# Performance work log

Hardware: AMD Instinct MI355X
Metric: run time of the kernel (lower is better)

The kernel has to match this reference:

```python
import jax, jax.numpy as jnp
import numpy as np


def mT(x):
    return jnp.swapaxes(x, -1, -2)


def bmv(A, x):
    # batched matrix-vector with broadcasting over leading dims
    return jnp.einsum('...mn,...n->...m', A, x)


def tri_inv(chol):
    # inverse of a batched lower-triangular matrix
    n = chol.shape[-1]
    I = jnp.broadcast_to(jnp.eye(n, dtype=chol.dtype), chol.shape)
    return jax.scipy.linalg.solve_triangular(chol, I, lower=True)


def chol_solve(Psi, v):
    # (chol chol^T)^{-1} v where Psi = inv(chol)^T  =>  Psi Psi^T v
    return bmv(Psi, bmv(mT(Psi), v))


def setup_inputs() -> dict:
    T, S, B, L, r = 500, 32, 128, 64, 8
    key = jax.random.key(0)
    ks = jax.random.split(key, 11)
    m_0 = jax.random.normal(ks[0], (L,), dtype=jnp.float32)
    Q_0_diag = 0.1 + 0.9 * jax.random.uniform(ks[1], (L,), dtype=jnp.float32)
    Q_diag = 0.1 + 0.9 * jax.random.uniform(ks[2], (L,), dtype=jnp.float32)
    k = 0.1 * jax.random.normal(ks[3], (T, B, L), dtype=jnp.float32)
    K = 0.3 * jax.random.normal(ks[4], (T, B, L, r), dtype=jnp.float32)
    A = jax.random.normal(ks[5], (L, L), dtype=jnp.float32) / jnp.sqrt(jnp.float32(L))
    w_p0 = jax.random.normal(ks[6], (S, B, L), dtype=jnp.float32)
    w_f0 = jax.random.normal(ks[7], (S, B, r), dtype=jnp.float32)
    w_p1 = jax.random.normal(ks[8], (T - 1, S, B, S), dtype=jnp.float32)
    w_p2 = jax.random.normal(ks[9], (T - 1, S, B, L), dtype=jnp.float32)
    w_f = jax.random.normal(ks[10], (T - 1, S, B, r), dtype=jnp.float32)
    return dict(m_0=m_0, Q_0_diag=Q_0_diag, Q_diag=Q_diag, k=k, K=K, A=A,
                w_p0=w_p0, w_f0=w_f0, w_p1=w_p1, w_p2=w_p2, w_f=w_f)


def reference(m_0, Q_0_diag, Q_diag, k, K, A, w_p0, w_f0, w_p1, w_p2, w_f):
    S = w_p0.shape[0]
    r = K.shape[-1]
    Qi = 1.0 / Q_diag
    Qs = jnp.sqrt(Q_diag)
    I_r = jnp.eye(r, dtype=K.dtype)
    I_S = jnp.eye(S, dtype=K.dtype)
    sqrt_S_inv = 1.0 / jnp.sqrt(jnp.asarray(S, K.dtype))

    def dyn(z):  # nonlinear dynamics mean fn (stand-in): residual tanh network
        return z + 0.1 * jnp.tanh(z @ A.T)

    # ---- fast_filter_step_0 ----
    Pp = Q_0_diag                               # initial predictive cov diag [L]
    z_p_c = jnp.sqrt(Pp) * w_p0                 # [S,B,L]
    h_p = jnp.broadcast_to(m_0 / Pp, k[0].shape)  # J_p m_p, [B,L]
    h = h_p + k[0]
    P_p_K = Pp[None, :, None] * K[0]            # [B,L,r]
    KPK = jnp.einsum('blr,bls->brs', K[0], P_p_K)
    Psi0 = mT(tri_inv(jnp.linalg.cholesky(I_r + KPK)))
    m0f = Pp * h - bmv(P_p_K, chol_solve(Psi0, bmv(mT(P_p_K), h)))
    v1 = bmv(mT(K[0]), z_p_c) + w_f0            # [S,B,r]
    z0 = m0f + z_p_c - Pp * bmv(K[0], chol_solve(Psi0, v1))

    # ---- fast_filter_step_t over t = 1..T-1 ----
    def step(z_f, xs):
        k_t, K_t, wp1, wp2, wf = xs
        # predict
        mth = jnp.moveaxis(dyn(z_f), 0, -1)     # [B,L,S]
        m_p = mth.mean(-1)                      # [B,L]
        M_c = sqrt_S_inv * (mth - m_p[..., None])  # [B,L,S]
        G = (mT(M_c) * Qi) @ M_c                # [B,S,S]
        Psi_p = mT(tri_inv(jnp.linalg.cholesky(I_S + G)))
        u1 = Qi * m_p
        h_p = u1 - Qi * bmv(M_c, chol_solve(Psi_p, bmv(mT(M_c), u1)))  # J_p m_p
        z_p_c = bmv(M_c, wp1) + Qs * wp2        # [S,B,L]
        # update
        h = h_p + k_t
        KM = mT(K_t) @ M_c                      # [B,r,S]
        KQ = mT(K_t) * Qs                       # [B,r,L]
        KPK_t = KM @ mT(KM) + KQ @ mT(KQ)
        Psi_f = mT(tri_inv(jnp.linalg.cholesky(I_r + KPK_t)))

        def P_p_mv(v):
            return bmv(M_c, bmv(mT(M_c), v)) + Q_diag * v

        u = P_p_mv(h)
        m_f = u - P_p_mv(bmv(K_t, chol_solve(Psi_f, bmv(mT(K_t), u))))
        v1t = bmv(mT(K_t), z_p_c) + wf
        z = m_f + z_p_c - P_p_mv(bmv(K_t, chol_solve(Psi_f, v1t)))
        return z, m_f

    _, m_rest = jax.lax.scan(step, z0, (k[1:], K[1:], w_p1, w_p2, w_f))
    return jnp.concatenate([m0f[None], m_rest], axis=0)  # [T,B,L]
```

## Files before the change

kernel.cpp:

```cpp
#include <hip/hip_runtime.h>
#include <hip/hip_bf16.h>
#include <cstdint>
#include <cstddef>

namespace {
constexpr int T_ = 500, S_ = 32, B_ = 128, L_ = 64, R_ = 8;

typedef __attribute__((ext_vector_type(8))) short short8;
typedef __attribute__((ext_vector_type(4))) float f32x4;

__device__ __forceinline__ float rdlane(float v, int l) {
  return __int_as_float(__builtin_amdgcn_readlane(__float_as_int(v), l));
}
template<int CTRL, int RM>
__device__ __forceinline__ float dppadd(float v) {
  int t = __builtin_amdgcn_update_dpp(0, __float_as_int(v), CTRL, RM, 0xf, false);
  return v + __int_as_float(t);
}
__device__ __forceinline__ float wredsum(float v) {
  v = dppadd<0x111, 0xf>(v);
  v = dppadd<0x112, 0xf>(v);
  v = dppadd<0x114, 0xf>(v);
  v = dppadd<0x118, 0xf>(v);
  v = dppadd<0x142, 0xa>(v);
  v = dppadd<0x143, 0xc>(v);
  return v;
}
__device__ __forceinline__ float wsum(float v) {
  v += __shfl_xor(v, 1);  v += __shfl_xor(v, 2);  v += __shfl_xor(v, 4);
  v += __shfl_xor(v, 8);  v += __shfl_xor(v, 16); v += __shfl_xor(v, 32);
  return v;
}
__device__ __forceinline__ void gload16(const float* g, float* l) {
  __builtin_amdgcn_global_load_lds((const __attribute__((address_space(1))) uint32_t*)g,
                                   (__attribute__((address_space(3))) uint32_t*)l,
                                   16, 0, 0);
}
__device__ __forceinline__ void bar_lgkm() {
  asm volatile("s_waitcnt lgkmcnt(0)\n\ts_barrier" ::: "memory");
}
__device__ __forceinline__ void fsplit(const float (&v)[8], short8& hi, short8& lo) {
#pragma unroll
  for (int j = 0; j < 8; ++j) {
    uint32_t u = __float_as_uint(v[j]);
    hi[j] = (short)(u >> 16);
    float hf = __uint_as_float(u & 0xFFFF0000u);
    float lf = v[j] - hf;
    lo[j] = (short)(__float_as_uint(lf) >> 16);
  }
}
__device__ __forceinline__ void ldfragF(const float* p, short8& hi, short8& lo) {
  float4 a = *(const float4*)p, b = *(const float4*)(p + 4);
  float v[8] = {a.x,a.y,a.z,a.w,b.x,b.y,b.z,b.w};
  fsplit(v, hi, lo);
}
__device__ __forceinline__ f32x4 mfma3(short8 ah, short8 al, short8 bh, short8 bl,
                                       f32x4 acc) {
  acc = __builtin_amdgcn_mfma_f32_16x16x32_bf16(ah, bh, acc, 0, 0, 0);
  acc = __builtin_amdgcn_mfma_f32_16x16x32_bf16(al, bh, acc, 0, 0, 0);
  acc = __builtin_amdgcn_mfma_f32_16x16x32_bf16(ah, bl, acc, 0, 0, 0);
  return acc;
}
}

__global__ __launch_bounds__(512, 1) void nlf_kernel(
    const float* __restrict__ m0p, const float* __restrict__ q0p,
    const float* __restrict__ qp,  const float* __restrict__ kp,
    const float* __restrict__ Kp,  const float* __restrict__ Ap,
    const float* __restrict__ wp0p, const float* __restrict__ wf0p,
    const float* __restrict__ wp1p, const float* __restrict__ wp2p,
    const float* __restrict__ wfp,  float* __restrict__ outp)
{
  __shared__ __align__(16) float z_s[S_*68];
  __shared__ __align__(16) float zn_s[S_*68];
  __shared__ __align__(16) float Mc_s[L_*36];
  __shared__ __align__(16) short McH_s[L_*40];
  __shared__ __align__(16) short McL_s[L_*40];
  __shared__ __align__(16) short McTH_s[S_*72];
  __shared__ __align__(16) short McTL_s[S_*72];
  __shared__ __align__(16) short KtTH_s[R_*72];
  __shared__ __align__(16) short KtTL_s[R_*72];
  __shared__ __align__(16) float uni[8*68];
  __shared__ __align__(16) float wp1b[2][S_*S_];
  __shared__ __align__(16) float wp2b[2][S_*L_];
  __shared__ __align__(16) float wf_s[S_*R_];
  __shared__ __align__(16) float Ktb[2][L_*R_];
  __shared__ __align__(16) float KtT_s[R_*68];
  __shared__ __align__(16) float ktv_s[L_];
  __shared__ __align__(16) float v1t_s[S_*R_];
  __shared__ __align__(16) float KM_s[S_*R_];
  __shared__ __align__(16) float mkm_s[L_*R_];
  __shared__ __align__(16) float M8_s[64];
  __shared__ __align__(16) float C8_s[64];
  __shared__ __align__(16) float tk_s[S_];
  __shared__ __align__(16) float mf_s[L_];
  __shared__ __align__(16) float qv_s[L_];
  __shared__ __align__(16) float qsv_s[L_];
  __shared__ __align__(16) float q0v_s[L_];

  const int tid = threadIdx.x;
  const int lam = tid & 63;
  const int w   = tid >> 6;
  const int b   = blockIdx.x;
  const int mtl = w >> 2, ntl = w & 3;
  const int cc  = lam & 15, gg = lam >> 4;

  const float q_r  = qp[lam];
  const float qs_r = sqrtf(q_r);
  const float q0_r = q0p[lam];
  const float m0_r = m0p[lam];
  if (tid < 64) { qv_s[tid] = q_r; qsv_s[tid] = qs_r; q0v_s[tid] = q0_r; }

  short8 ABh[2], ABl[2];
  {
    const float* arow = Ap + (size_t)(ntl*16 + cc)*64;
#pragma unroll
    for (int kk = 0; kk < 2; ++kk)
      ldfragF(arow + kk*32 + gg*8, ABh[kk], ABl[kk]);
  }

  float Kreg[8];
  {
    const float* kb = Kp + (size_t)b*(L_*R_) + lam*R_;
    float4 ka = *(const float4*)kb, kb4 = *(const float4*)(kb+4);
    Kreg[0]=ka.x;Kreg[1]=ka.y;Kreg[2]=ka.z;Kreg[3]=ka.w;
    Kreg[4]=kb4.x;Kreg[5]=kb4.y;Kreg[6]=kb4.z;Kreg[7]=kb4.w;
  }
  float kt_r = kp[(size_t)b*L_ + lam];

  if (w == 0) {
#pragma unroll
    for (int m = 0; m < 4; ++m) {
      int f = m*256 + lam*4, s = f >> 5, c = f & 31;
      gload16(wp1p + ((size_t)s*B_ + b)*S_ + c, &wp1b[1][f]);
    }
  } else if (w == 1 || w == 2) {
#pragma unroll
    for (int m = 0; m < 4; ++m) {
      int f = (w-1)*1024 + m*256 + lam*4, s = f >> 6, c = f & 63;
      gload16(wp2p + ((size_t)s*B_ + b)*L_ + c, &wp2b[1][f]);
    }
  } else if (w == 3) {
    { int f = lam*4, s = f >> 3, c = f & 7;
      gload16(wf0p + ((size_t)s*B_ + b)*R_ + c, &wf_s[f]); }
#pragma unroll
    for (int m = 0; m < 2; ++m) {
      int f = m*256 + lam*4;
      gload16(Kp + (size_t)b*(L_*R_) + f, &Ktb[0][f]);
    }
  } else if (w == 4 || w == 5) {
#pragma unroll
    for (int m = 0; m < 4; ++m) {
      int f = (w-4)*1024 + m*256 + lam*4, s = f >> 6, c = f & 63;
      gload16(wp0p + ((size_t)s*B_ + b)*L_ + c, &wp2b[0][f]);
    }
  } else if (w == 6) {
#pragma unroll
    for (int m = 0; m < 2; ++m) {
      int f = m*256 + lam*4;
      gload16(Kp + ((size_t)1*B_ + b)*(L_*R_) + f, &Ktb[1][f]);
    }
  }
  __syncthreads();

  auto chol8M8 = [&]() {
    const int i8 = lam & 7;
    float c8[8], rd8 = 0.0f;
#pragma unroll
    for (int k = 0; k < 8; ++k) c8[k] = C8_s[i8*8 + k];
#pragma unroll
    for (int j = 0; j < 8; ++j) {
      float dj = rdlane(c8[j], j);
      float rinv = rsqrtf(dj);
      if (i8 == j) rd8 = rinv;
      c8[j] *= rinv;
#pragma unroll
      for (int k = j+1; k < 8; ++k)
        c8[k] = fmaf(-rdlane(c8[j], k), c8[j], c8[k]);
    }
    float w8[8];
#pragma unroll
    for (int i = 0; i < 8; ++i) {
      float sacc = (i == i8) ? 1.0f : 0.0f;
#pragma unroll
      for (int k = 0; k < i; ++k)
        sacc = fmaf(-rdlane(c8[k], i), w8[k], sacc);
      w8[i] = sacc * rdlane(rd8, i);
    }
#pragma unroll
    for (int i = 0; i < 8; ++i) {
      float msum = 0.0f;
#pragma unroll
      for (int k = 0; k < 8; ++k)
        msum = fmaf(rdlane(w8[k], i), w8[k], msum);
      if (lam < 8) M8_s[i*8 + lam] = msum;
    }
  };

  {
    const float Pp = q0_r;
    const float h0 = m0_r / Pp + kt_r;
    if (w == 0) {
      const int r1 = lam >> 3, r2 = lam & 7;
      float acc = 0.0f;
#pragma unroll 4
      for (int l = 0; l < 64; ++l)
        acc = fmaf(Ktb[0][l*8 + r1] * q0v_s[l], Ktb[0][l*8 + r2], acc);
      C8_s[lam] = acc + (r1 == r2 ? 1.0f : 0.0f);
      chol8M8();
      float t8[8];
#pragma unroll
      for (int r = 0; r < 8; ++r) t8[r] = wsum(Pp * Kreg[r] * h0);
      float acc2 = 0.0f;
#pragma unroll
      for (int r1i = 0; r1i < 8; ++r1i) {
        float4 ma = *(const float4*)&M8_s[r1i*8];
        float4 mb = *(const float4*)&M8_s[r1i*8+4];
        float y = ma.x*t8[0]+ma.y*t8[1]+ma.z*t8[2]+ma.w*t8[3]
                + mb.x*t8[4]+mb.y*t8[5]+mb.z*t8[6]+mb.w*t8[7];
        acc2 = fmaf(Kreg[r1i], y, acc2);
      }
      float m0f = Pp*h0 - Pp*acc2;
      mf_s[lam] = m0f;
      outp[(size_t)b*L_ + lam] = m0f;
    }
    __syncthreads();

    const float qs0 = sqrtf(q0_r);
#pragma unroll
    for (int i = 0; i < 4; ++i) {
      const int s = 4*w + i;
      float zp = qs0 * wp2b[0][s*64 + lam];
      float v1[8];
#pragma unroll
      for (int r = 0; r < 8; ++r)
        v1[r] = wsum(Kreg[r] * zp) + wf_s[s*8 + r];
      float acc = 0.0f;
#pragma unroll
      for (int r1i = 0; r1i < 8; ++r1i) {
        float4 ma = *(const float4*)&M8_s[r1i*8];
        float4 mb = *(const float4*)&M8_s[r1i*8+4];
        float y = ma.x*v1[0]+ma.y*v1[1]+ma.z*v1[2]+ma.w*v1[3]
                + mb.x*v1[4]+mb.y*v1[5]+mb.z*v1[6]+mb.w*v1[7];
        acc = fmaf(Kreg[r1i], y, acc);
      }
      z_s[s*68 + lam] = zp - Pp*acc;
    }
  }
  __syncthreads();

  for (int t = 1; t < T_; ++t) {
    const int cb = t & 1, nb = cb ^ 1;

    {
      const float* kb = Kp + ((size_t)t*B_ + b)*(L_*R_) + lam*R_;
      float4 ka = *(const float4*)kb, kb4 = *(const float4*)(kb+4);
      Kreg[0]=ka.x;Kreg[1]=ka.y;Kreg[2]=ka.z;Kreg[3]=ka.w;
      Kreg[4]=kb4.x;Kreg[5]=kb4.y;Kreg[6]=kb4.z;Kreg[7]=kb4.w;
      kt_r = kp[((size_t)t*B_ + b)*L_ + lam];
    }
    if (w == 0) ktv_s[lam] = kt_r;

    {
      f32x4 acc = {0.0f, 0.0f, 0.0f, 0.0f};
#pragma unroll
      for (int kk = 0; kk < 2; ++kk) {
        const int l0 = kk*32 + gg*8;
        const int row = mtl*16 + cc;
        float4 za = *(const float4*)&z_s[row*68 + l0];
        float4 zb = *(const float4*)&z_s[row*68 + l0 + 4];
        float4 ma4 = *(const float4*)&mf_s[l0];
        float4 mb4 = *(const float4*)&mf_s[l0 + 4];
        float z8[8] = {za.x+ma4.x, za.y+ma4.y, za.z+ma4.z, za.w+ma4.w,
                       zb.x+mb4.x, zb.y+mb4.y, zb.z+mb4.z, zb.w+mb4.w};
        short8 ah, al;
        fsplit(z8, ah, al);
        acc = __builtin_amdgcn_mfma_f32_16x16x32_bf16(ah, ABh[kk], acc, 0, 0, 0);
        acc = __builtin_amdgcn_mfma_f32_16x16x32_bf16(al, ABh[kk], acc, 0, 0, 0);
        acc = __builtin_amdgcn_mfma_f32_16x16x32_bf16(ah, ABl[kk], acc, 0, 0, 0);
      }
      const int lout = ntl*16 + cc;
      const float mfl = mf_s[lout];
      float psum = 0.0f;
#pragma unroll
      for (int r = 0; r < 4; ++r) {
        const int sr = mtl*16 + gg*4 + r;
        float x = acc[r];
        float e = __expf(2.0f*x);
        float tnh = 1.0f - 2.0f/(e + 1.0f);
        float zv = (z_s[sr*68 + lout] + mfl) + 0.1f*tnh;
        zn_s[sr*68 + lout] = zv;
        psum += zv;
      }
      uni[(mtl*4 + gg)*68 + lout] = psum;
    }
    bar_lgkm();

    if (w == 0) {
      if (t < T_-1) {
#pragma unroll
        for (int m = 0; m < 4; ++m) {
          int f = m*256 + lam*4, s = f >> 5, c = f & 31;
          gload16(wp1p + (((size_t)t*S_ + s)*B_ + b)*S_ + c, &wp1b[nb][f]);
        }
      }
    } else if (w == 1 || w == 2) {
      if (t < T_-1) {
#pragma unroll
        for (int m = 0; m < 4; ++m) {
          int f = (w-1)*1024 + m*256 + lam*4, s = f >> 6, c = f & 63;
          gload16(wp2p + (((size_t)t*S_ + s)*B_ + b)*L_ + c, &wp2b[nb][f]);
        }
      }
    } else if (w == 3) {
      { int f = lam*4, s = f >> 3, c = f & 7;
        gload16(wfp + (((size_t)(t-1)*S_ + s)*B_ + b)*R_ + c, &wf_s[f]); }
      if (t < T_-1) {
#pragma unroll
        for (int m = 0; m < 2; ++m) {
          int f = m*256 + lam*4;
          gload16(Kp + ((size_t)(t+1)*B_ + b)*(L_*R_) + f, &Ktb[nb][f]);
        }
      }
    }

    float mp = 0.0f;
#pragma unroll
    for (int ww = 0; ww < 8; ++ww) mp += uni[ww*68 + lam];
    mp *= 0.03125f;
    {
      short h4[4], l4[4];
#pragma unroll
      for (int i = 0; i < 4; ++i) {
        const int s = 4*w + i;
        float mcv = (zn_s[s*68 + lam] - mp) * 0.17677669529663689f;
        Mc_s[lam*36 + s] = mcv;
        uint32_t u = __float_as_uint(mcv);
        short hs = (short)(u >> 16);
        float hf = __uint_as_float(u & 0xFFFF0000u);
        short ls = (short)(__float_as_uint(mcv - hf) >> 16);
        h4[i] = hs; l4[i] = ls;
        McTH_s[s*72 + lam] = hs;
        McTL_s[s*72 + lam] = ls;
      }
      uint32_t hp0 = (uint32_t)(uint16_t)h4[0] | ((uint32_t)(uint16_t)h4[1] << 16);
      uint32_t hp1 = (uint32_t)(uint16_t)h4[2] | ((uint32_t)(uint16_t)h4[3] << 16);
      uint32_t lp0 = (uint32_t)(uint16_t)l4[0] | ((uint32_t)(uint16_t)l4[1] << 16);
      uint32_t lp1 = (uint32_t)(uint16_t)l4[2] | ((uint32_t)(uint16_t)l4[3] << 16);
      *(uint2*)&McH_s[lam*40 + 4*w] = make_uint2(hp0, hp1);
      *(uint2*)&McL_s[lam*40 + 4*w] = make_uint2(lp0, lp1);
    }
    if (w == 5) {
      float4 a = *(const float4*)&Ktb[cb][lam*8];
      float4 c4 = *(const float4*)&Ktb[cb][lam*8+4];
      float kv[8] = {a.x,a.y,a.z,a.w,c4.x,c4.y,c4.z,c4.w};
#pragma unroll
      for (int r = 0; r < 8; ++r) {
        KtT_s[r*68 + lam] = kv[r];
        uint32_t u = __float_as_uint(kv[r]);
        short hs = (short)(u >> 16);
        float hf = __uint_as_float(u & 0xFFFF0000u);
        short ls = (short)(__float_as_uint(kv[r] - hf) >> 16);
        KtTH_s[r*72 + lam] = hs;
        KtTL_s[r*72 + lam] = ls;
      }
    }
    __syncthreads();

    if (w >= 2) {
      auto zpTile = [&](int tl) {
        const int mt = tl >> 2, nt = tl & 3;
        short8 ah, al;
        ldfragF(&wp1b[cb][(mt*16+cc)*32 + gg*8], ah, al);
        short8 bh = *(const short8*)&McH_s[(nt*16+cc)*40 + gg*8];
        short8 bl = *(const short8*)&McL_s[(nt*16+cc)*40 + gg*8];
        f32x4 acc = {0,0,0,0};
        acc = mfma3(ah, al, bh, bl, acc);
        const int col = nt*16 + cc;
        const float qsc = qsv_s[col];
#pragma unroll
        for (int r = 0; r < 4; ++r) {
          const int row = mt*16 + gg*4 + r;
          zn_s[row*68 + col] = acc[r] + qsc * wp2b[cb][row*64 + col];
        }
      };
      if (w <= 5) zpTile(w - 2);
      else { zpTile(2*w - 8); zpTile(2*w - 7); }
    } else {
      const int mt = w;
      f32x4 acc = {0,0,0,0};
#pragma unroll
      for (int ks = 0; ks < 2; ++ks) {
        short8 ah = *(const short8*)&McTH_s[(mt*16+cc)*72 + ks*32 + gg*8];
        short8 al = *(const short8*)&McTL_s[(mt*16+cc)*72 + ks*32 + gg*8];
        short8 bh, bl;
        if (cc < 8) {
          bh = *(const short8*)&KtTH_s[cc*72 + ks*32 + gg*8];
          bl = *(const short8*)&KtTL_s[cc*72 + ks*32 + gg*8];
        } else if (cc == 8) {
          float bv[8];
#pragma unroll
          for (int j = 0; j < 8; ++j) bv[j] = ktv_s[ks*32 + gg*8 + j];
          fsplit(bv, bh, bl);
        } else {
          bh = short8{0,0,0,0,0,0,0,0}; bl = short8{0,0,0,0,0,0,0,0};
        }
        acc = mfma3(ah, al, bh, bl, acc);
      }
#pragma unroll
      for (int r = 0; r < 4; ++r) {
        const int s = mt*16 + gg*4 + r;
        if (cc < 8) KM_s[s*8 + cc] = acc[r];
        else if (cc == 8) tk_s[s] = acc[r];
      }
    }
    bar_lgkm();

    float u_r = 0.0f, t8s[8];
#pragma unroll
    for (int r = 0; r < 8; ++r) t8s[r] = 0.0f;
    if (w == 0) {
      float mctk = 0.0f;
#pragma unroll
      for (int s4 = 0; s4 < 32; s4 += 4) {
        float4 mc4 = *(const float4*)&Mc_s[lam*36 + s4];
        float4 tb  = *(const float4*)&tk_s[s4];
        mctk = fmaf(mc4.x, tb.x, mctk);
        mctk = fmaf(mc4.y, tb.y, mctk);
        mctk = fmaf(mc4.z, tb.z, mctk);
        mctk = fmaf(mc4.w, tb.w, mctk);
      }
      u_r = mp + mctk + q_r * kt_r;
#pragma unroll
      for (int r = 0; r < 8; ++r)
        t8s[r] = rdlane(wredsum(Kreg[r] * u_r), 63);
    } else if (w == 1) {
      const int r1 = lam >> 3, r2 = lam & 7;
      float acc = 0.0f;
#pragma unroll 4
      for (int s = 0; s < 32; ++s)
        acc = fmaf(KM_s[s*8 + r1], KM_s[s*8 + r2], acc);
#pragma unroll 4
      for (int l4 = 0; l4 < 64; l4 += 4) {
        float4 ka = *(const float4*)&KtT_s[r1*68 + l4];
        float4 kb = *(const float4*)&KtT_s[r2*68 + l4];
        float4 qv4 = *(const float4*)&qv_s[l4];
        acc = fmaf(ka.x*qv4.x, kb.x, acc);
        acc = fmaf(ka.y*qv4.y, kb.y, acc);
        acc = fmaf(ka.z*qv4.z, kb.z, acc);
        acc = fmaf(ka.w*qv4.w, kb.w, acc);
      }
      C8_s[lam] = acc + (r1 == r2 ? 1.0f : 0.0f);
      chol8M8();
    } else if (w == 2 || w == 3) {
      const int mt = w - 2;
      f32x4 acc = {0,0,0,0};
#pragma unroll
      for (int ks = 0; ks < 2; ++ks) {
        short8 ah, al;
        ldfragF(&zn_s[(mt*16+cc)*68 + ks*32 + gg*8], ah, al);
        short8 bh, bl;
        if (cc < 8) {
          bh = *(const short8*)&KtTH_s[cc*72 + ks*32 + gg*8];
          bl = *(const short8*)&KtTL_s[cc*72 + ks*32 + gg*8];
        } else {
          bh = short8{0,0,0,0,0,0,0,0}; bl = short8{0,0,0,0,0,0,0,0};
        }
        acc = mfma3(ah, al, bh, bl, acc);
      }
#pragma unroll
      for (int r = 0; r < 4; ++r) {
        const int s = mt*16 + gg*4 + r;
        if (cc < 8) v1t_s[s*8 + cc] = acc[r] + wf_s[s*8 + cc];
      }
    } else if (w == 4) {
      float mkm[8];
#pragma unroll
      for (int r = 0; r < 8; ++r) mkm[r] = 0.0f;
#pragma unroll
      for (int s4 = 0; s4 < 32; s4 += 4) {
        float4 mc4 = *(const float4*)&Mc_s[lam*36 + s4];
#pragma unroll
        for (int ii = 0; ii < 4; ++ii) {
          const float mcl = (ii==0)?mc4.x:(ii==1)?mc4.y:(ii==2)?mc4.z:mc4.w;
          float4 ka = *(const float4*)&KM_s[(s4+ii)*8];
          float4 kb = *(const float4*)&KM_s[(s4+ii)*8+4];
          mkm[0] = fmaf(mcl, ka.x, mkm[0]);
          mkm[1] = fmaf(mcl, ka.y, mkm[1]);
          mkm[2] = fmaf(mcl, ka.z, mkm[2]);
          mkm[3] = fmaf(mcl, ka.w, mkm[3]);
          mkm[4] = fmaf(mcl, kb.x, mkm[4]);
          mkm[5] = fmaf(mcl, kb.y, mkm[5]);
          mkm[6] = fmaf(mcl, kb.z, mkm[6]);
          mkm[7] = fmaf(mcl, kb.w, mkm[7]);
        }
      }
      *(float4*)&mkm_s[lam*8]   = make_float4(mkm[0],mkm[1],mkm[2],mkm[3]);
      *(float4*)&mkm_s[lam*8+4] = make_float4(mkm[4],mkm[5],mkm[6],mkm[7]);
    }
    bar_lgkm();

    float4 mk_a = *(const float4*)&mkm_s[lam*8];
    float4 mk_b = *(const float4*)&mkm_s[lam*8+4];
    const float mkmv[8] = {mk_a.x, mk_a.y, mk_a.z, mk_a.w,
                           mk_b.x, mk_b.y, mk_b.z, mk_b.w};
    float kM8[8], mkmM8[8];
#pragma unroll
    for (int j = 0; j < 8; ++j) { kM8[j] = 0.0f; mkmM8[j] = 0.0f; }
#pragma unroll
    for (int r = 0; r < 8; ++r) {
      float4 ma = *(const float4*)&M8_s[r*8];
      float4 mb = *(const float4*)&M8_s[r*8+4];
      const float kr = Kreg[r], mr = mkmv[r];
      kM8[0] = fmaf(kr, ma.x, kM8[0]);   mkmM8[0] = fmaf(mr, ma.x, mkmM8[0]);
      kM8[1] = fmaf(kr, ma.y, kM8[1]);   mkmM8[1] = fmaf(mr, ma.y, mkmM8[1]);
      kM8[2] = fmaf(kr, ma.z, kM8[2]);   mkmM8[2] = fmaf(mr, ma.z, mkmM8[2]);
      kM8[3] = fmaf(kr, ma.w, kM8[3]);   mkmM8[3] = fmaf(mr, ma.w, mkmM8[3]);
      kM8[4] = fmaf(kr, mb.x, kM8[4]);   mkmM8[4] = fmaf(mr, mb.x, mkmM8[4]);
      kM8[5] = fmaf(kr, mb.y, kM8[5]);   mkmM8[5] = fmaf(mr, mb.y, mkmM8[5]);
      kM8[6] = fmaf(kr, mb.z, kM8[6]);   mkmM8[6] = fmaf(mr, mb.z, mkmM8[6]);
      kM8[7] = fmaf(kr, mb.w, kM8[7]);   mkmM8[7] = fmaf(mr, mb.w, mkmM8[7]);
    }
#pragma unroll
    for (int i = 0; i < 4; ++i) {
      const int s = 4*w + i;
      float4 va = *(const float4*)&v1t_s[s*8];
      float4 vb = *(const float4*)&v1t_s[s*8+4];
      float g    = kM8[0]*va.x + kM8[1]*va.y + kM8[2]*va.z + kM8[3]*va.w
                 + kM8[4]*vb.x + kM8[5]*vb.y + kM8[6]*vb.z + kM8[7]*vb.w;
      float corr = mkmM8[0]*va.x + mkmM8[1]*va.y + mkmM8[2]*va.z + mkmM8[3]*va.w
                 + mkmM8[4]*vb.x + mkmM8[5]*vb.y + mkmM8[6]*vb.z + mkmM8[7]*vb.w;
      float zp = zn_s[s*68 + lam];
      z_s[s*68 + lam] = zp - corr - q_r*g;
    }
    if (w == 0) {
      float g    = kM8[0]*t8s[0] + kM8[1]*t8s[1] + kM8[2]*t8s[2] + kM8[3]*t8s[3]
                 + kM8[4]*t8s[4] + kM8[5]*t8s[5] + kM8[6]*t8s[6] + kM8[7]*t8s[7];
      float corr = mkmM8[0]*t8s[0] + mkmM8[1]*t8s[1] + mkmM8[2]*t8s[2] + mkmM8[3]*t8s[3]
                 + mkmM8[4]*t8s[4] + mkmM8[5]*t8s[5] + mkmM8[6]*t8s[6] + mkmM8[7]*t8s[7];
      const float mf_r = u_r - corr - q_r*g;
      mf_s[lam] = mf_r;
      outp[((size_t)t*B_ + b)*L_ + lam] = mf_r;
    }
    bar_lgkm();
  }
}

extern "C" void kernel_launch(void* const* d_in, const int* in_sizes, int n_in,
                              void* d_out, int out_size, void* d_ws, size_t ws_size,
                              hipStream_t stream) {
  (void)in_sizes; (void)n_in; (void)out_size; (void)d_ws; (void)ws_size;
  nlf_kernel<<<dim3(B_), dim3(512), 0, stream>>>(
      (const float*)d_in[0], (const float*)d_in[1], (const float*)d_in[2],
      (const float*)d_in[3], (const float*)d_in[4], (const float*)d_in[5],
      (const float*)d_in[6], (const float*)d_in[7], (const float*)d_in[8],
      (const float*)d_in[9], (const float*)d_in[10], (float*)d_out);
}
```

Measured before the change: 2.670 ms.

## Move next-step prefetch after barrier, double-buffer wf, transpose KM for vector loads

The global-to-LDS prefetch of the next step's noise and K tiles is moved later in the step, after a cheaper lgkm-only barrier replaces a full __syncthreads. The wf buffer is now double-buffered so it can be loaded a step ahead like the other inputs, and the end-of-step barrier now waits on vmcnt so these loads are complete. KM is also written in transposed form so the Gram accumulation uses float4 LDS reads instead of scalar strided ones. The trade-off is a stricter end-of-step wait on global loads plus a little extra LDS and store traffic.

After: 2.581 ms. 3.3% less time.

```diff
diff --git a/kernel.cpp b/kernel.cpp
--- a/kernel.cpp
+++ b/kernel.cpp
@@ -38,6 +38,9 @@
 }
 __device__ __forceinline__ void bar_lgkm() {
   asm volatile("s_waitcnt lgkmcnt(0)\n\ts_barrier" ::: "memory");
+}
+__device__ __forceinline__ void barV() {
+  asm volatile("s_waitcnt vmcnt(0) lgkmcnt(0)\n\ts_barrier" ::: "memory");
 }
 __device__ __forceinline__ void fsplit(const float (&v)[8], short8& hi, short8& lo) {
 #pragma unroll
@@ -83,12 +86,13 @@
   __shared__ __align__(16) float uni[8*68];
   __shared__ __align__(16) float wp1b[2][S_*S_];
   __shared__ __align__(16) float wp2b[2][S_*L_];
-  __shared__ __align__(16) float wf_s[S_*R_];
+  __shared__ __align__(16) float wfb[2][S_*R_];
   __shared__ __align__(16) float Ktb[2][L_*R_];
   __shared__ __align__(16) float KtT_s[R_*68];
   __shared__ __align__(16) float ktv_s[L_];
   __shared__ __align__(16) float v1t_s[S_*R_];
   __shared__ __align__(16) float KM_s[S_*R_];
+  __shared__ __align__(16) float KMT_s[R_*36];
   __shared__ __align__(16) float mkm_s[L_*R_];
   __shared__ __align__(16) float M8_s[64];
   __shared__ __align__(16) float C8_s[64];
@@ -142,7 +146,7 @@
     }
   } else if (w == 3) {
     { int f = lam*4, s = f >> 3, c = f & 7;
-      gload16(wf0p + ((size_t)s*B_ + b)*R_ + c, &wf_s[f]); }
+      gload16(wf0p + ((size_t)s*B_ + b)*R_ + c, &wfb[0][f]); }
 #pragma unroll
     for (int m = 0; m < 2; ++m) {
       int f = m*256 + lam*4;
@@ -160,6 +164,9 @@
       int f = m*256 + lam*4;
       gload16(Kp + ((size_t)1*B_ + b)*(L_*R_) + f, &Ktb[1][f]);
     }
+  } else if (w == 7) {
+    int f = lam*4, s = f >> 3, c = f & 7;
+    gload16(wfp + ((size_t)s*B_ + b)*R_ + c, &wfb[1][f]);
   }
   __syncthreads();
 
@@ -234,7 +241,7 @@
       float v1[8];
 #pragma unroll
       for (int r = 0; r < 8; ++r)
-        v1[r] = wsum(Kreg[r] * zp) + wf_s[s*8 + r];
+        v1[r] = wsum(Kreg[r] * zp) + wfb[0][s*8 + r];
       float acc = 0.0f;
 #pragma unroll
       for (int r1i = 0; r1i < 8; ++r1i) {
@@ -296,34 +303,6 @@
     }
     bar_lgkm();
 
-    if (w == 0) {
-      if (t < T_-1) {
-#pragma unroll
-        for (int m = 0; m < 4; ++m) {
-          int f = m*256 + lam*4, s = f >> 5, c = f & 31;
-          gload16(wp1p + (((size_t)t*S_ + s)*B_ + b)*S_ + c, &wp1b[nb][f]);
-        }
-      }
-    } else if (w == 1 || w == 2) {
-      if (t < T_-1) {
-#pragma unroll
-        for (int m = 0; m < 4; ++m) {
-          int f = (w-1)*1024 + m*256 + lam*4, s = f >> 6, c = f & 63;
-          gload16(wp2p + (((size_t)t*S_ + s)*B_ + b)*L_ + c, &wp2b[nb][f]);
-        }
-      }
-    } else if (w == 3) {
-      { int f = lam*4, s = f >> 3, c = f & 7;
-        gload16(wfp + (((size_t)(t-1)*S_ + s)*B_ + b)*R_ + c, &wf_s[f]); }
-      if (t < T_-1) {
-#pragma unroll
-        for (int m = 0; m < 2; ++m) {
-          int f = m*256 + lam*4;
-          gload16(Kp + ((size_t)(t+1)*B_ + b)*(L_*R_) + f, &Ktb[nb][f]);
-        }
-      }
-    }
-
     float mp = 0.0f;
 #pragma unroll
     for (int ww = 0; ww < 8; ++ww) mp += uni[ww*68 + lam];
@@ -365,7 +344,31 @@
         KtTL_s[r*72 + lam] = ls;
       }
     }
-    __syncthreads();
+    bar_lgkm();
+
+    if (t < T_-1) {
+      if (w == 0) {
+#pragma unroll
+        for (int m = 0; m < 4; ++m) {
+          int f = m*256 + lam*4, s = f >> 5, c = f & 31;
+          gload16(wp1p + (((size_t)t*S_ + s)*B_ + b)*S_ + c, &wp1b[nb][f]);
+        }
+      } else if (w == 1 || w == 2) {
+#pragma unroll
+        for (int m = 0; m < 4; ++m) {
+          int f = (w-1)*1024 + m*256 + lam*4, s = f >> 6, c = f & 63;
+          gload16(wp2p + (((size_t)t*S_ + s)*B_ + b)*L_ + c, &wp2b[nb][f]);
+        }
+      } else if (w == 3) {
+        { int f = lam*4, s = f >> 3, c = f & 7;
+          gload16(wfp + (((size_t)t*S_ + s)*B_ + b)*R_ + c, &wfb[nb][f]); }
+#pragma unroll
+        for (int m = 0; m < 2; ++m) {
+          int f = m*256 + lam*4;
+          gload16(Kp + ((size_t)(t+1)*B_ + b)*(L_*R_) + f, &Ktb[nb][f]);
+        }
+      }
+    }
 
     if (w >= 2) {
       auto zpTile = [&](int tl) {
@@ -410,7 +413,7 @@
 #pragma unroll
       for (int r = 0; r < 4; ++r) {
         const int s = mt*16 + gg*4 + r;
-        if (cc < 8) KM_s[s*8 + cc] = acc[r];
+        if (cc < 8) { KM_s[s*8 + cc] = acc[r]; KMT_s[cc*36 + s] = acc[r]; }
         else if (cc == 8) tk_s[s] = acc[r];
       }
     }
@@ -437,9 +440,15 @@
     } else if (w == 1) {
       const int r1 = lam >> 3, r2 = lam & 7;
       float acc = 0.0f;
-#pragma unroll 4
-      for (int s = 0; s < 32; ++s)
-        acc = fmaf(KM_s[s*8 + r1], KM_s[s*8 + r2], acc);
+#pragma unroll
+      for (int s4 = 0; s4 < 32; s4 += 4) {
+        float4 ka = *(const float4*)&KMT_s[r1*36 + s4];
+        float4 kb = *(const float4*)&KMT_s[r2*36 + s4];
+        acc = fmaf(ka.x, kb.x, acc);
+        acc = fmaf(ka.y, kb.y, acc);
+        acc = fmaf(ka.z, kb.z, acc);
+        acc = fmaf(ka.w, kb.w, acc);
+      }
 #pragma unroll 4
       for (int l4 = 0; l4 < 64; l4 += 4) {
         float4 ka = *(const float4*)&KtT_s[r1*68 + l4];
@@ -471,7 +480,7 @@
 #pragma unroll
       for (int r = 0; r < 4; ++r) {
         const int s = mt*16 + gg*4 + r;
-        if (cc < 8) v1t_s[s*8 + cc] = acc[r] + wf_s[s*8 + cc];
+        if (cc < 8) v1t_s[s*8 + cc] = acc[r] + wfb[cb][s*8 + cc];
       }
     } else if (w == 4) {
       float mkm[8];
@@ -542,7 +551,7 @@
       mf_s[lam] = mf_r;
       outp[((size_t)t*B_ + b)*L_ + lam] = mf_r;
     }
-    bar_lgkm();
+    barV();
   }
 }
 
```
